# Performance work log

Hardware: AMD Instinct MI355X
Metric: run time of the kernel (lower is better)

## Reference

```python
import jax, jax.numpy as jnp
import numpy as np

N_JOINTS = 50
N_BONES = 50  # mask slicing [:, :, :50] / [:, :, :150] in the source requires exactly 50 bones
# Original repo's getSkeletalModelStructure() is not provided; use deterministic
# bone pairs (i, (i+1) % 50) over the 50 joints. Same gather+norm+direction math.
BONE_A = np.arange(N_JOINTS)
BONE_B = (BONE_A + 1) % N_JOINTS


def _length_direct(x):
    # x: [B, T, 150] -> joints [B, T, 50, 3]
    B, T, _ = x.shape
    joints = x.reshape(B, T, N_JOINTS, 3)
    diff = joints[:, :, BONE_A, :] - joints[:, :, BONE_B, :]  # [B, T, 50, 3]
    length = jnp.linalg.norm(diff, axis=-1)                   # [B, T, 50]
    tiny = jnp.finfo(x.dtype).tiny
    direct = diff / (length[..., None] + tiny)                # [B, T, 50, 3]
    return length, direct.reshape(B, T, N_BONES * 3)          # [B, T, 150]


def setup_inputs() -> dict:
    key = jax.random.key(0)
    k1, k2 = jax.random.split(key)
    shape = (128, 1024, 150)
    return {
        "preds": jax.random.normal(k1, shape, dtype=jnp.float32),
        "targets": jax.random.normal(k2, shape, dtype=jnp.float32),
    }


def reference(preds, targets):
    target_pad = 0.0
    loss_scale = 0.1
    mask = (targets != target_pad).astype(preds.dtype)  # [B, T, 150]
    p = preds * mask
    t = targets * mask
    # lengths are computed in the original but unused in the final loss;
    # only the direction terms enter the bone loss.
    _, p_dir = _length_direct(p)
    _, t_dir = _length_direct(t)
    p_dir = p_dir * mask[:, :, :150]
    t_dir = t_dir * mask[:, :, :150]
    loss = jnp.mean(jnp.abs(p - t)) + 0.1 * jnp.mean((p_dir - t_dir) ** 2)
    return loss * loss_scale
```

## Files before the change

### kernel.cpp

```cpp
#include <hip/hip_runtime.h>

constexpr int      FRAMES  = 128 * 1024;
constexpr int      FRAME_F = 150;
constexpr unsigned NT      = (unsigned)FRAMES * 50u;
constexpr float    SCALE   = 0.1f / ((float)FRAMES * (float)FRAME_F);

constexpr int      BLOCK   = 256;
constexpr int      NBLK    = 2048;
constexpr unsigned STRIDE  = (unsigned)BLOCK * NBLK;
constexpr int      FULL    = NT / STRIDE;

__device__ __forceinline__ float bone_term(const float* __restrict__ ps,
                                           const float* __restrict__ ts,
                                           int no)
{
    const float* pn = ps + no;
    const float* tn = ts + no;

    const float p0 = ps[0], p1 = ps[1], p2 = ps[2];
    const float t0 = ts[0], t1 = ts[1], t2 = ts[2];
    const float q0 = pn[0], q1 = pn[1], q2 = pn[2];
    const float u0 = tn[0], u1 = tn[1], u2 = tn[2];

    const float m0 = (t0 != 0.0f) ? 1.0f : 0.0f;
    const float m1 = (t1 != 0.0f) ? 1.0f : 0.0f;
    const float m2 = (t2 != 0.0f) ? 1.0f : 0.0f;
    const float n0 = (u0 != 0.0f) ? 1.0f : 0.0f;
    const float n1 = (u1 != 0.0f) ? 1.0f : 0.0f;
    const float n2 = (u2 != 0.0f) ? 1.0f : 0.0f;

    const float pm0 = p0 * m0, pm1 = p1 * m1, pm2 = p2 * m2;
    const float qm0 = q0 * n0, qm1 = q1 * n1, qm2 = q2 * n2;

    const float ab = fabsf(pm0 - t0) + fabsf(pm1 - t1) + fabsf(pm2 - t2);

    const float pd0 = pm0 - qm0, pd1 = pm1 - qm1, pd2 = pm2 - qm2;
    const float td0 = t0 - u0,   td1 = t1 - u1,   td2 = t2 - u2;

    const float pl2 = pd0*pd0 + pd1*pd1 + pd2*pd2;
    const float tl2 = td0*td0 + td1*td1 + td2*td2;
    const float pri = (pl2 > 0.0f) ? __builtin_amdgcn_rsqf(pl2) : 0.0f;
    const float tri = (tl2 > 0.0f) ? __builtin_amdgcn_rsqf(tl2) : 0.0f;

    const float d0 = pd0 * pri - td0 * tri;
    const float d1 = pd1 * pri - td1 * tri;
    const float d2 = pd2 * pri - td2 * tri;
    const float sq = m0*d0*d0 + m1*d1*d1 + m2*d2*d2;

    return ab + 0.1f * sq;
}

__global__ __launch_bounds__(BLOCK, 4) void bone_loss_main(
    const float* __restrict__ preds,
    const float* __restrict__ targets,
    float* __restrict__ partials)
{
    const unsigned g  = blockIdx.x * BLOCK + threadIdx.x;
    const unsigned j0 = g % 50u;

    float acc = 0.0f;

    #pragma unroll
    for (int b = 0; b < FULL; ++b) {
        const unsigned kb  = 49u - (38u * (unsigned)b) % 50u;
        const int      no  = (j0 == kb) ? (3 - FRAME_F) : 3;
        const size_t   e   = (size_t)(g + (unsigned)b * STRIDE) * 3u;
        acc += bone_term(preds + e, targets + e, no);
    }

    {
        const unsigned idx = g + (unsigned)FULL * STRIDE;
        if (idx < NT) {
            const unsigned kb = 49u - (38u * (unsigned)FULL) % 50u;
            const int      no = (j0 == kb) ? (3 - FRAME_F) : 3;
            const size_t   e  = (size_t)idx * 3u;
            acc += bone_term(preds + e, targets + e, no);
        }
    }

    #pragma unroll
    for (int off = 32; off > 0; off >>= 1)
        acc += __shfl_down(acc, off, 64);

    __shared__ float ws[4];
    const int wid = threadIdx.x >> 6;
    if ((threadIdx.x & 63) == 0) ws[wid] = acc;
    __syncthreads();
    if (threadIdx.x == 0)
        partials[blockIdx.x] = ws[0] + ws[1] + ws[2] + ws[3];
}

__global__ __launch_bounds__(256) void bone_loss_finish(
    const float* __restrict__ partials,
    float* __restrict__ out)
{
    float v = 0.0f;
    for (int i = threadIdx.x; i < NBLK; i += 256)
        v += partials[i];

    #pragma unroll
    for (int off = 32; off > 0; off >>= 1)
        v += __shfl_down(v, off, 64);

    __shared__ float ws[4];
    const int wid = threadIdx.x >> 6;
    if ((threadIdx.x & 63) == 0) ws[wid] = v;
    __syncthreads();
    if (threadIdx.x == 0)
        out[0] = (ws[0] + ws[1] + ws[2] + ws[3]) * SCALE;
}

extern "C" void kernel_launch(void* const* d_in, const int* in_sizes, int n_in,
                              void* d_out, int out_size, void* d_ws, size_t ws_size,
                              hipStream_t stream) {
    const float* preds   = (const float*)d_in[0];
    const float* targets = (const float*)d_in[1];
    float* out      = (float*)d_out;
    float* partials = (float*)d_ws;

    bone_loss_main<<<NBLK, BLOCK, 0, stream>>>(preds, targets, partials);
    bone_loss_finish<<<1, 256, 0, stream>>>(partials, out);
}
```

Before: 178.0 us.

## Process eight consecutive joints per thread with float4 vector loads

Each thread now handles a contiguous chunk of 8 joints (24 floats) and loads them with six float4 loads per tensor, instead of one joint per thread with scalar strided loads. The neighbour joint is reused from registers, with one extra scalar load for the chunk's end and the wraparound joint. The grid shrinks to 1600 blocks so that two chunks per thread cover the data exactly. This aims to cut load instruction count and redundant neighbour fetches, at the cost of higher register pressure and less coalesced per-lane access patterns.

```diff
diff --git a/kernel.cpp b/kernel.cpp
--- a/kernel.cpp
+++ b/kernel.cpp
@@ -6,22 +6,15 @@
 constexpr float    SCALE   = 0.1f / ((float)FRAMES * (float)FRAME_F);
 
 constexpr int      BLOCK   = 256;
-constexpr int      NBLK    = 2048;
-constexpr unsigned STRIDE  = (unsigned)BLOCK * NBLK;
-constexpr int      FULL    = NT / STRIDE;
+constexpr int      NBLK    = 1600;
+constexpr int      TPT     = 8;
+constexpr unsigned NCHUNK  = NT / TPT;
+constexpr unsigned CSTRIDE = (unsigned)NBLK * BLOCK;
 
-__device__ __forceinline__ float bone_term(const float* __restrict__ ps,
-                                           const float* __restrict__ ts,
-                                           int no)
+__device__ __forceinline__ float bone_term(
+    float p0, float p1, float p2, float t0, float t1, float t2,
+    float q0, float q1, float q2, float u0, float u1, float u2)
 {
-    const float* pn = ps + no;
-    const float* tn = ts + no;
-
-    const float p0 = ps[0], p1 = ps[1], p2 = ps[2];
-    const float t0 = ts[0], t1 = ts[1], t2 = ts[2];
-    const float q0 = pn[0], q1 = pn[1], q2 = pn[2];
-    const float u0 = tn[0], u1 = tn[1], u2 = tn[2];
-
     const float m0 = (t0 != 0.0f) ? 1.0f : 0.0f;
     const float m1 = (t1 != 0.0f) ? 1.0f : 0.0f;
     const float m2 = (t2 != 0.0f) ? 1.0f : 0.0f;
@@ -50,33 +43,60 @@
     return ab + 0.1f * sq;
 }
 
+__device__ __forceinline__ float chunk8(const float* __restrict__ preds,
+                                        const float* __restrict__ targets,
+                                        unsigned chunk)
+{
+    const unsigned bt = chunk * (unsigned)TPT;
+    const unsigned j0 = bt % 50u;
+    const float* P = preds   + (size_t)bt * 3u;
+    const float* T = targets + (size_t)bt * 3u;
+
+    const int eoff = (j0 == 42u) ? 0 : TPT * 3;
+    const int woff = (j0 >= 42u) ? -(int)(3u * j0) : 0;
+
+    float p[27], t[27], pw[3], tw[3];
+    const float4* P4 = reinterpret_cast<const float4*>(P);
+    const float4* T4 = reinterpret_cast<const float4*>(T);
+    #pragma unroll
+    for (int i = 0; i < 6; ++i) {
+        const float4 a = P4[i];
+        p[4*i+0] = a.x; p[4*i+1] = a.y; p[4*i+2] = a.z; p[4*i+3] = a.w;
+        const float4 b = T4[i];
+        t[4*i+0] = b.x; t[4*i+1] = b.y; t[4*i+2] = b.z; t[4*i+3] = b.w;
+    }
+    p[24] = P[eoff+0]; p[25] = P[eoff+1]; p[26] = P[eoff+2];
+    t[24] = T[eoff+0]; t[25] = T[eoff+1]; t[26] = T[eoff+2];
+    pw[0] = P[woff+0]; pw[1] = P[woff+1]; pw[2] = P[woff+2];
+    tw[0] = T[woff+0]; tw[1] = T[woff+1]; tw[2] = T[woff+2];
+
+    float acc = 0.0f;
+    #pragma unroll
+    for (int k = 0; k < TPT; ++k) {
+        const bool w = (j0 == 49u - (unsigned)k);
+        const int  n = 3 * (k + 1);
+        const float q0 = w ? pw[0] : p[n+0];
+        const float q1 = w ? pw[1] : p[n+1];
+        const float q2 = w ? pw[2] : p[n+2];
+        const float u0 = w ? tw[0] : t[n+0];
+        const float u1 = w ? tw[1] : t[n+1];
+        const float u2 = w ? tw[2] : t[n+2];
+        acc += bone_term(p[3*k+0], p[3*k+1], p[3*k+2],
+                         t[3*k+0], t[3*k+1], t[3*k+2],
+                         q0, q1, q2, u0, u1, u2);
+    }
+    return acc;
+}
+
 __global__ __launch_bounds__(BLOCK, 4) void bone_loss_main(
     const float* __restrict__ preds,
     const float* __restrict__ targets,
     float* __restrict__ partials)
 {
-    const unsigned g  = blockIdx.x * BLOCK + threadIdx.x;
-    const unsigned j0 = g % 50u;
+    const unsigned th = blockIdx.x * BLOCK + threadIdx.x;
 
-    float acc = 0.0f;
-
-    #pragma unroll
-    for (int b = 0; b < FULL; ++b) {
-        const unsigned kb  = 49u - (38u * (unsigned)b) % 50u;
-        const int      no  = (j0 == kb) ? (3 - FRAME_F) : 3;
-        const size_t   e   = (size_t)(g + (unsigned)b * STRIDE) * 3u;
-        acc += bone_term(preds + e, targets + e, no);
-    }
-
-    {
-        const unsigned idx = g + (unsigned)FULL * STRIDE;
-        if (idx < NT) {
-            const unsigned kb = 49u - (38u * (unsigned)FULL) % 50u;
-            const int      no = (j0 == kb) ? (3 - FRAME_F) : 3;
-            const size_t   e  = (size_t)idx * 3u;
-            acc += bone_term(preds + e, targets + e, no);
-        }
-    }
+    float acc = chunk8(preds, targets, th)
+              + chunk8(preds, targets, th + CSTRIDE);
 
     #pragma unroll
     for (int off = 32; off > 0; off >>= 1)
```

Result: slower. 202.1 us (+13.5%).

## Process four joints per thread with float4 vector loads

Applied to the files above, without the earlier changes.

Each thread now handles a chunk of four consecutive joints (12 floats), loading them as three float4 vectors per tensor instead of scalar strided loads. Neighbor joints come from the same registers, with extra scalar loads only for the next chunk's first joint and the frame wraparound case. This is meant to cut load instruction count and redundant neighbor reads while keeping coalesced wide accesses. The cost is more registers per thread, and the per-thread stride of 48 bytes may hurt coalescing.

```diff
diff --git a/kernel.cpp b/kernel.cpp
--- a/kernel.cpp
+++ b/kernel.cpp
@@ -7,21 +7,15 @@
 
 constexpr int      BLOCK   = 256;
 constexpr int      NBLK    = 2048;
-constexpr unsigned STRIDE  = (unsigned)BLOCK * NBLK;
-constexpr int      FULL    = NT / STRIDE;
+constexpr unsigned G       = (unsigned)NBLK * BLOCK;
+constexpr unsigned NC      = NT / 4u;
+constexpr int      FULL    = (int)(NC / G);
+constexpr unsigned TAILN   = NC - (unsigned)FULL * G;
 
-__device__ __forceinline__ float bone_term(const float* __restrict__ ps,
-                                           const float* __restrict__ ts,
-                                           int no)
+__device__ __forceinline__ float bone_term(
+    float p0, float p1, float p2, float t0, float t1, float t2,
+    float q0, float q1, float q2, float u0, float u1, float u2)
 {
-    const float* pn = ps + no;
-    const float* tn = ts + no;
-
-    const float p0 = ps[0], p1 = ps[1], p2 = ps[2];
-    const float t0 = ts[0], t1 = ts[1], t2 = ts[2];
-    const float q0 = pn[0], q1 = pn[1], q2 = pn[2];
-    const float u0 = tn[0], u1 = tn[1], u2 = tn[2];
-
     const float m0 = (t0 != 0.0f) ? 1.0f : 0.0f;
     const float m1 = (t1 != 0.0f) ? 1.0f : 0.0f;
     const float m2 = (t2 != 0.0f) ? 1.0f : 0.0f;
@@ -50,33 +44,57 @@
     return ab + 0.1f * sq;
 }
 
+__device__ __forceinline__ float chunk4(const float* __restrict__ preds,
+                                        const float* __restrict__ targets,
+                                        unsigned c)
+{
+    const unsigned bt = c * 4u;
+    const unsigned j0 = bt % 50u;
+    const float* P = preds   + (size_t)bt * 3u;
+    const float* T = targets + (size_t)bt * 3u;
+
+    const int eoff = (j0 == 46u) ? 0 : 12;
+    const int woff = (j0 == 48u) ? -144 : (j0 == 46u) ? -138 : 0;
+
+    const float4 pa = *reinterpret_cast<const float4*>(P + 0);
+    const float4 pb = *reinterpret_cast<const float4*>(P + 4);
+    const float4 pc = *reinterpret_cast<const float4*>(P + 8);
+    const float4 ta = *reinterpret_cast<const float4*>(T + 0);
+    const float4 tb = *reinterpret_cast<const float4*>(T + 4);
+    const float4 tc = *reinterpret_cast<const float4*>(T + 8);
+    const float ps0 = P[eoff+0], ps1 = P[eoff+1], ps2 = P[eoff+2];
+    const float ts0 = T[eoff+0], ts1 = T[eoff+1], ts2 = T[eoff+2];
+    const float pw0 = P[woff+0], pw1 = P[woff+1], pw2 = P[woff+2];
+    const float tw0 = T[woff+0], tw1 = T[woff+1], tw2 = T[woff+2];
+
+    const bool w1 = (j0 == 48u);
+    const bool w3 = (j0 == 46u);
+
+    float acc = bone_term(pa.x, pa.y, pa.z,  ta.x, ta.y, ta.z,
+                          pa.w, pb.x, pb.y,  ta.w, tb.x, tb.y);
+    acc += bone_term(pa.w, pb.x, pb.y,  ta.w, tb.x, tb.y,
+                     w1 ? pw0 : pb.z, w1 ? pw1 : pb.w, w1 ? pw2 : pc.x,
+                     w1 ? tw0 : tb.z, w1 ? tw1 : tb.w, w1 ? tw2 : tc.x);
+    acc += bone_term(pb.z, pb.w, pc.x,  tb.z, tb.w, tc.x,
+                     pc.y, pc.z, pc.w,  tc.y, tc.z, tc.w);
+    acc += bone_term(pc.y, pc.z, pc.w,  tc.y, tc.z, tc.w,
+                     w3 ? pw0 : ps0, w3 ? pw1 : ps1, w3 ? pw2 : ps2,
+                     w3 ? tw0 : ts0, w3 ? tw1 : ts1, w3 ? tw2 : ts2);
+    return acc;
+}
+
 __global__ __launch_bounds__(BLOCK, 4) void bone_loss_main(
     const float* __restrict__ preds,
     const float* __restrict__ targets,
     float* __restrict__ partials)
 {
-    const unsigned g  = blockIdx.x * BLOCK + threadIdx.x;
-    const unsigned j0 = g % 50u;
+    const unsigned tid = blockIdx.x * BLOCK + threadIdx.x;
 
-    float acc = 0.0f;
-
-    #pragma unroll
-    for (int b = 0; b < FULL; ++b) {
-        const unsigned kb  = 49u - (38u * (unsigned)b) % 50u;
-        const int      no  = (j0 == kb) ? (3 - FRAME_F) : 3;
-        const size_t   e   = (size_t)(g + (unsigned)b * STRIDE) * 3u;
-        acc += bone_term(preds + e, targets + e, no);
-    }
-
-    {
-        const unsigned idx = g + (unsigned)FULL * STRIDE;
-        if (idx < NT) {
-            const unsigned kb = 49u - (38u * (unsigned)FULL) % 50u;
-            const int      no = (j0 == kb) ? (3 - FRAME_F) : 3;
-            const size_t   e  = (size_t)idx * 3u;
-            acc += bone_term(preds + e, targets + e, no);
-        }
-    }
+    float acc = chunk4(preds, targets, tid);
+    acc += chunk4(preds, targets, tid + G);
+    acc += chunk4(preds, targets, tid + 2u * G);
+    if (tid < TAILN)
+        acc += chunk4(preds, targets, tid + 3u * G);
 
     #pragma unroll
     for (int off = 32; off > 0; off >>= 1)
```

Measured after the change: 204.4 us. 1.15x slower.

## Stage frames through double-buffered LDS with async global_load_lds pipeline

Applied to the files above, without the earlier changes.

Replaces direct strided per-thread global loads with coalesced 16-byte global_load_lds copies of 16-frame chunks into double-buffered shared memory. The next chunk's load is issued while the current chunk is computed, with manual vmcnt waits and barriers. Neighbor-joint reads then come from LDS rather than overlapping global reads. It adds barrier overhead and LDS bank conflicts from stride-3 access, and relies on hand-tuned waitcnt values being correct per wave.

```diff
diff --git a/kernel.cpp b/kernel.cpp
--- a/kernel.cpp
+++ b/kernel.cpp
@@ -1,27 +1,25 @@
 #include <hip/hip_runtime.h>
 
-constexpr int      FRAMES  = 128 * 1024;
-constexpr int      FRAME_F = 150;
-constexpr unsigned NT      = (unsigned)FRAMES * 50u;
-constexpr float    SCALE   = 0.1f / ((float)FRAMES * (float)FRAME_F);
+constexpr int   FRAMES  = 128 * 1024;
+constexpr int   FRAME_F = 150;
+constexpr float SCALE   = 0.1f / ((float)FRAMES * (float)FRAME_F);
 
-constexpr int      BLOCK   = 256;
-constexpr int      NBLK    = 2048;
-constexpr unsigned STRIDE  = (unsigned)BLOCK * NBLK;
-constexpr int      FULL    = NT / STRIDE;
+constexpr int BLOCK    = 256;
+constexpr int SFRAMES  = 16;
+constexpr int STRIPLES = SFRAMES * 50;
+constexpr int SFLOATS  = SFRAMES * FRAME_F;
+constexpr int SSEGS    = SFLOATS / 4;
+constexpr int NBLK     = 1024;
+constexpr int NSTAGES  = FRAMES / SFRAMES;
+constexpr int SPB      = NSTAGES / NBLK;
 
-__device__ __forceinline__ float bone_term(const float* __restrict__ ps,
-                                           const float* __restrict__ ts,
-                                           int no)
+typedef __attribute__((address_space(1))) const void  gvoid;
+typedef __attribute__((address_space(3)))       void  lvoid;
+
+__device__ __forceinline__ float bone_term(
+    float p0, float p1, float p2, float t0, float t1, float t2,
+    float q0, float q1, float q2, float u0, float u1, float u2)
 {
-    const float* pn = ps + no;
-    const float* tn = ts + no;
-
-    const float p0 = ps[0], p1 = ps[1], p2 = ps[2];
-    const float t0 = ts[0], t1 = ts[1], t2 = ts[2];
-    const float q0 = pn[0], q1 = pn[1], q2 = pn[2];
-    const float u0 = tn[0], u1 = tn[1], u2 = tn[2];
-
     const float m0 = (t0 != 0.0f) ? 1.0f : 0.0f;
     const float m1 = (t1 != 0.0f) ? 1.0f : 0.0f;
     const float m2 = (t2 != 0.0f) ? 1.0f : 0.0f;
@@ -50,32 +48,86 @@
     return ab + 0.1f * sq;
 }
 
+__device__ __forceinline__ void stage_issue(const float4* __restrict__ gp,
+                                            const float4* __restrict__ gt,
+                                            float4* lp, float4* lt,
+                                            int wid, int lane)
+{
+    #pragma unroll
+    for (int it = 0; it < 3; ++it) {
+        const int segb = it * 256 + wid * 64;
+        const int seg  = segb + lane;
+        if (seg < SSEGS) {
+            __builtin_amdgcn_global_load_lds((gvoid*)(gp + seg), (lvoid*)(lp + segb), 16, 0, 0);
+            __builtin_amdgcn_global_load_lds((gvoid*)(gt + seg), (lvoid*)(lt + segb), 16, 0, 0);
+        }
+    }
+}
+
+__device__ __forceinline__ float compute_stage(const float* __restrict__ lp,
+                                               const float* __restrict__ lt,
+                                               int tid, int j0)
+{
+    float acc = 0.0f;
+    #pragma unroll
+    for (int it = 0; it < 4; ++it) {
+        const int idx = it * 256 + tid;
+        if (idx < STRIPLES) {
+            int j = j0 + (it * 256) % 50;
+            if (j >= 50) j -= 50;
+            const int nidx = (j == 49) ? idx - 49 : idx + 1;
+            const int s = idx * 3, n = nidx * 3;
+            acc += bone_term(lp[s+0], lp[s+1], lp[s+2],
+                             lt[s+0], lt[s+1], lt[s+2],
+                             lp[n+0], lp[n+1], lp[n+2],
+                             lt[n+0], lt[n+1], lt[n+2]);
+        }
+    }
+    return acc;
+}
+
 __global__ __launch_bounds__(BLOCK, 4) void bone_loss_main(
     const float* __restrict__ preds,
     const float* __restrict__ targets,
     float* __restrict__ partials)
 {
-    const unsigned g  = blockIdx.x * BLOCK + threadIdx.x;
-    const unsigned j0 = g % 50u;
+    __shared__ float4 ldsP[2][SSEGS];
+    __shared__ float4 ldsT[2][SSEGS];
+
+    const int tid  = threadIdx.x;
+    const int wid  = tid >> 6;
+    const int lane = tid & 63;
+    const int j0   = tid % 50;
+    const int s0   = blockIdx.x * SPB;
+
+    const float4* gp = reinterpret_cast<const float4*>(preds);
+    const float4* gt = reinterpret_cast<const float4*>(targets);
+
+    stage_issue(gp + (size_t)s0 * SSEGS, gt + (size_t)s0 * SSEGS,
+                ldsP[0], ldsT[0], wid, lane);
 
     float acc = 0.0f;
+    for (int i = 0; i < SPB; ++i) {
+        const int c = i & 1;
 
-    #pragma unroll
-    for (int b = 0; b < FULL; ++b) {
-        const unsigned kb  = 49u - (38u * (unsigned)b) % 50u;
-        const int      no  = (j0 == kb) ? (3 - FRAME_F) : 3;
-        const size_t   e   = (size_t)(g + (unsigned)b * STRIDE) * 3u;
-        acc += bone_term(preds + e, targets + e, no);
-    }
+        if (i + 1 < SPB)
+            stage_issue(gp + (size_t)(s0 + i + 1) * SSEGS,
+                        gt + (size_t)(s0 + i + 1) * SSEGS,
+                        ldsP[c ^ 1], ldsT[c ^ 1], wid, lane);
 
-    {
-        const unsigned idx = g + (unsigned)FULL * STRIDE;
-        if (idx < NT) {
-            const unsigned kb = 49u - (38u * (unsigned)FULL) % 50u;
-            const int      no = (j0 == kb) ? (3 - FRAME_F) : 3;
-            const size_t   e  = (size_t)idx * 3u;
-            acc += bone_term(preds + e, targets + e, no);
+        if (i + 1 < SPB) {
+            if (wid < 2) asm volatile("s_waitcnt vmcnt(6)" ::: "memory");
+            else         asm volatile("s_waitcnt vmcnt(4)" ::: "memory");
+        } else {
+            asm volatile("s_waitcnt vmcnt(0)" ::: "memory");
         }
+        __builtin_amdgcn_s_barrier();
+        asm volatile("" ::: "memory");
+
+        acc += compute_stage((const float*)ldsP[c], (const float*)ldsT[c], tid, j0);
+
+        asm volatile("" ::: "memory");
+        __builtin_amdgcn_s_barrier();
     }
 
     #pragma unroll
@@ -83,10 +135,9 @@
         acc += __shfl_down(acc, off, 64);
 
     __shared__ float ws[4];
-    const int wid = threadIdx.x >> 6;
-    if ((threadIdx.x & 63) == 0) ws[wid] = acc;
+    if (lane == 0) ws[wid] = acc;
     __syncthreads();
-    if (threadIdx.x == 0)
+    if (tid == 0)
         partials[blockIdx.x] = ws[0] + ws[1] + ws[2] + ws[3];
 }
 
```

New measurement: 178.1 us. No clear change (+0.0%).
